# Performance work log

Hardware: AMD Instinct MI355X
Metric: run time of the kernel (lower is better)

## Reference

```python
import jax, jax.numpy as jnp
import numpy as np

D_MODEL = 1024
NUM_HEADS = 16
WINDOW = 128
DISP = WINDOW // 2
SHIFTED = True
NEG = -9e15


def _create_mask(w):
    # 1 = keep, 0 = masked; zero top-right and bottom-left DISP blocks
    m = np.ones((w, w), dtype=np.float32)
    m[:DISP, -DISP:] = 0.0
    m[-DISP:, :DISP] = 0.0
    return jnp.asarray(m)


def setup_inputs() -> dict:
    key = jax.random.key(0)
    ks = jax.random.split(key, 5)
    b, s, d = 4, 8192, D_MODEL
    sc = 1.0 / np.sqrt(d)
    return {
        "x": jax.random.normal(ks[0], (b, s, d), jnp.float32),
        "w_qkv": jax.random.normal(ks[1], (d, 3 * d), jnp.float32) * sc,
        "b_qkv": jax.random.normal(ks[2], (3 * d,), jnp.float32) * 0.02,
        "w_o": jax.random.normal(ks[3], (d, d), jnp.float32) * sc,
        "b_o": jax.random.normal(ks[4], (d,), jnp.float32) * 0.02,
    }


def reference(x, w_qkv, b_qkv, w_o, b_o):
    b, s, d = x.shape
    h, w = NUM_HEADS, WINDOW
    d_k = d // h
    if SHIFTED:
        x = jnp.roll(x, -DISP, axis=1)
    xw = x.reshape(-1, w, d)                       # (n, w, d), n = b*s/w
    n = xw.shape[0]
    qkv = xw @ w_qkv + b_qkv                       # (n, w, 3d)
    # replicate torch rearrange 'n w (h d_k qkv) -> n h w (d_k qkv)' + chunk(3)
    qkv = qkv.reshape(n, w, h, d_k, 3)             # split (h d_k qkv)
    qkv = qkv.transpose(0, 2, 1, 3, 4).reshape(n, h, w, 3 * d_k)
    q, k, v = jnp.split(qkv, 3, axis=-1)           # each (n, h, w, d_k)
    attn = jnp.einsum('nhqd,nhkd->nhqk', q, k) / jnp.sqrt(jnp.float32(d_k))
    if SHIFTED:
        mask = _create_mask(w)                     # (w, w)
        attn = jnp.where(mask == 0, jnp.float32(NEG), attn)
    attn = jax.nn.softmax(attn, axis=-1)
    vals = jnp.einsum('nhqk,nhkd->nhqd', attn, v)  # (n, h, w, d_k)
    vals = vals.transpose(0, 2, 1, 3).reshape(n, w, d)
    out = vals @ w_o + b_o                         # (n, w, d)
    out = out.reshape(b, s, d)
    if SHIFTED:
        out = jnp.roll(out, DISP, axis=1)
    return out
```

## Files before the change

### kernel.cpp

```cpp
#include <hip/hip_runtime.h>
#include <hip/hip_bf16.h>
#include <stdint.h>

#define D_MODEL   1024
#define SEQ       8192
#define BATCH     4
#define ROWS      (BATCH*SEQ)
#define NQKV      3072
#define HEADS     16
#define DKH       64

typedef _Float16 f16;
typedef f16   f16x8 __attribute__((ext_vector_type(8)));
typedef f16   f16x4 __attribute__((ext_vector_type(4)));
typedef float f32x4 __attribute__((ext_vector_type(4)));

#define AS1 __attribute__((address_space(1)))
#define AS3 __attribute__((address_space(3)))

__device__ __forceinline__ void lds_load16(const void* g, void* l) {
  __builtin_amdgcn_global_load_lds((const AS1 void*)g, (AS3 void*)l, 16, 0, 0);
}

__global__ void cvt_weights(const float* __restrict__ wqkv,
                            const float* __restrict__ bqkv,
                            const float* __restrict__ wo,
                            f16* __restrict__ wqkvT,
                            float* __restrict__ bqkvR,
                            f16* __restrict__ woT)
{
  const int NW1 = NQKV * D_MODEL;
  const int NW2 = D_MODEL * D_MODEL;
  int i = blockIdx.x * 256 + threadIdx.x;
  if (i < NW1) {
    int c = i % NQKV, k = i / NQKV;
    int hh = c / 192, rr = c % 192;
    int t  = rr >> 6, a = rr & 63;
    int n  = t * 1024 + hh * 64 + a;
    wqkvT[(size_t)n * 1024 + k] = (f16)wqkv[i];
  } else if (i < NW1 + NW2) {
    int j = i - NW1;
    int n = j % D_MODEL, k = j / D_MODEL;
    woT[(size_t)n * 1024 + k] = (f16)wo[j];
  } else if (i < NW1 + NW2 + NQKV) {
    int c = i - NW1 - NW2;
    int hh = c / 192, rr = c % 192;
    int t  = rr >> 6, a = rr & 63;
    bqkvR[t * 1024 + hh * 64 + a] = bqkv[c];
  }
}

__global__ void cvt_x(const float* __restrict__ x, f16* __restrict__ xb)
{
  int i  = blockIdx.x * 256 + threadIdx.x;
  int r  = i >> 7;
  int c8 = i & 127;
  int bb = r >> 13, p = r & 8191;
  int sr = (bb << 13) | ((p + 64) & 8191);
  const float* src = x + (size_t)sr * 1024 + c8 * 8;
  float4 v0 = *(const float4*)(src);
  float4 v1 = *(const float4*)(src + 4);
  f16x8 o = { (f16)v0.x, (f16)v0.y, (f16)v0.z, (f16)v0.w,
              (f16)v1.x, (f16)v1.y, (f16)v1.z, (f16)v1.w };
  *(f16x8*)(xb + (size_t)r * 1024 + c8 * 8) = o;
}

template<int EPI>
__global__ __launch_bounds__(256)
void gemm_bt(const f16* __restrict__ A, const f16* __restrict__ B,
             const float* __restrict__ bias,
             f16* __restrict__ outQ, f16* __restrict__ outK,
             f16* __restrict__ outVT, float* __restrict__ outF,
             int Ntiles)
{
  __shared__ alignas(16) char lds[32768];
  char* Asm = lds;
  char* Bsm = lds + 16384;

  int nwg  = gridDim.x;
  int cpx  = nwg >> 3;
  int work = (blockIdx.x & 7) * cpx + (blockIdx.x >> 3);
  int mt = work / Ntiles, nt = work % Ntiles;
  int m0 = mt * 128, n0 = nt * 128;

  int tid = threadIdx.x;
  int w = tid >> 6, l = tid & 63;
  int wr = w >> 1, wc = w & 1;
  int srow = l >> 3, sj = l & 7;
  int c16 = l & 15, g4 = l >> 4;

  const char* Ab = (const char*)A;
  const char* Bb = (const char*)B;

  f32x4 acc[4][4];
#pragma unroll
  for (int mi = 0; mi < 4; ++mi)
#pragma unroll
    for (int nj = 0; nj < 4; ++nj)
      acc[mi][nj] = (f32x4){0.f, 0.f, 0.f, 0.f};

  for (int kt = 0; kt < 16; ++kt) {
    int k0 = kt * 64;
#pragma unroll
    for (int q = 0; q < 4; ++q) {
      int r  = w * 32 + q * 8 + srow;
      int jg = sj ^ (r & 7);
      lds_load16(Ab + (size_t)(m0 + r) * 2048 + k0 * 2 + jg * 16,
                 Asm + (w * 32 + q * 8) * 128);
      lds_load16(Bb + (size_t)(n0 + r) * 2048 + k0 * 2 + jg * 16,
                 Bsm + (w * 32 + q * 8) * 128);
    }
    __syncthreads();
#pragma unroll
    for (int kk = 0; kk < 2; ++kk) {
      f16x8 af[4], bfr[4];
#pragma unroll
      for (int mi = 0; mi < 4; ++mi) {
        int r  = wr * 64 + mi * 16 + c16;
        int ch = ((kk << 2) | g4) ^ (r & 7);
        af[mi] = *(const f16x8*)(Asm + r * 128 + ch * 16);
      }
#pragma unroll
      for (int nj = 0; nj < 4; ++nj) {
        int r  = wc * 64 + nj * 16 + c16;
        int ch = ((kk << 2) | g4) ^ (r & 7);
        bfr[nj] = *(const f16x8*)(Bsm + r * 128 + ch * 16);
      }
#pragma unroll
      for (int mi = 0; mi < 4; ++mi)
#pragma unroll
        for (int nj = 0; nj < 4; ++nj)
          acc[mi][nj] = __builtin_amdgcn_mfma_f32_16x16x32_f16(
              af[mi], bfr[nj], acc[mi][nj], 0, 0, 0);
    }
    __syncthreads();
  }

  int rbase = g4 * 4;
  if (EPI == 0) {
    int tt = n0 >> 10;
#pragma unroll
    for (int mi = 0; mi < 4; ++mi) {
#pragma unroll
      for (int nj = 0; nj < 4; ++nj) {
        int n  = n0 + wc * 64 + nj * 16 + c16;
        int nn = n & 1023;
        float bv = bias[n];
#pragma unroll
        for (int j = 0; j < 4; ++j) {
          int m = m0 + wr * 64 + mi * 16 + rbase + j;
          float v = acc[mi][nj][j] + bv;
          if (tt == 0) {
            outQ[(size_t)m * 1024 + nn] = (f16)v;
          } else if (tt == 1) {
            outK[(size_t)m * 1024 + nn] = (f16)v;
          } else {
            int sub = m >> 6, key = m & 63;
            int hh = nn >> 6, dk = nn & 63;
            outVT[(((size_t)(sub * 16 + hh) * 64 + dk) << 6) + key] = (f16)v;
          }
        }
      }
    }
  } else {
#pragma unroll
    for (int mi = 0; mi < 4; ++mi) {
#pragma unroll
      for (int nj = 0; nj < 4; ++nj) {
        int n = n0 + wc * 64 + nj * 16 + c16;
        float bv = bias[n];
#pragma unroll
        for (int j = 0; j < 4; ++j) {
          int m = m0 + wr * 64 + mi * 16 + rbase + j;
          int bb = m >> 13, p = m & 8191;
          int dr = (bb << 13) | ((p + 64) & 8191);
          outF[(size_t)dr * 1024 + n] = acc[mi][nj][j] + bv;
        }
      }
    }
  }
}

__global__ __launch_bounds__(64)
void attn64(const f16* __restrict__ Q, const f16* __restrict__ Kb,
            const f16* __restrict__ VT, f16* __restrict__ O)
{
  __shared__ alignas(16) char plds[8192];
  int u = blockIdx.x;
  int sub = u >> 4, hh = u & 15;
  int l = threadIdx.x;
  int c = l & 15, g = l >> 4;

  const char* Qb = (const char*)Q  + (size_t)sub * 64 * 2048 + hh * 128;
  const char* KB = (const char*)Kb + (size_t)sub * 64 * 2048 + hh * 128;
  const char* VB = (const char*)VT + (size_t)u * 8192;

  f16x8 aq[4][2], bk[4][2];
#pragma unroll
  for (int mi = 0; mi < 4; ++mi)
#pragma unroll
    for (int kb = 0; kb < 2; ++kb)
      aq[mi][kb] = *(const f16x8*)(Qb + (mi * 16 + c) * 2048 + (kb * 32 + g * 8) * 2);
#pragma unroll
  for (int nj = 0; nj < 4; ++nj)
#pragma unroll
    for (int kb = 0; kb < 2; ++kb)
      bk[nj][kb] = *(const f16x8*)(KB + (nj * 16 + c) * 2048 + (kb * 32 + g * 8) * 2);

  f32x4 s[4][4];
#pragma unroll
  for (int mi = 0; mi < 4; ++mi)
#pragma unroll
    for (int nj = 0; nj < 4; ++nj)
      s[mi][nj] = (f32x4){0.f, 0.f, 0.f, 0.f};
#pragma unroll
  for (int kb = 0; kb < 2; ++kb)
#pragma unroll
    for (int mi = 0; mi < 4; ++mi)
#pragma unroll
      for (int nj = 0; nj < 4; ++nj)
        s[mi][nj] = __builtin_amdgcn_mfma_f32_16x16x32_f16(
            aq[mi][kb], bk[nj][kb], s[mi][nj], 0, 0, 0);

  const float SM_SCALE = 0.125f * 1.44269504089f;
#pragma unroll
  for (int mi = 0; mi < 4; ++mi) {
#pragma unroll
    for (int j = 0; j < 4; ++j) {
      float v0 = s[mi][0][j], v1 = s[mi][1][j], v2 = s[mi][2][j], v3 = s[mi][3][j];
      float mx = fmaxf(fmaxf(v0, v1), fmaxf(v2, v3));
      mx = fmaxf(mx, __shfl_xor(mx, 1));
      mx = fmaxf(mx, __shfl_xor(mx, 2));
      mx = fmaxf(mx, __shfl_xor(mx, 4));
      mx = fmaxf(mx, __shfl_xor(mx, 8));
      float p0 = exp2f((v0 - mx) * SM_SCALE);
      float p1 = exp2f((v1 - mx) * SM_SCALE);
      float p2 = exp2f((v2 - mx) * SM_SCALE);
      float p3 = exp2f((v3 - mx) * SM_SCALE);
      float sm = (p0 + p1) + (p2 + p3);
      sm += __shfl_xor(sm, 1);
      sm += __shfl_xor(sm, 2);
      sm += __shfl_xor(sm, 4);
      sm += __shfl_xor(sm, 8);
      float inv = 1.0f / sm;
      int r = mi * 16 + g * 4 + j;
      int rbyte = r * 128, rx = (r & 7) << 4;
      {
        int key = c;
        *(f16*)(plds + rbyte + (((key >> 3) << 4) ^ rx) + ((key & 7) << 1)) = (f16)(p0 * inv);
      }
      {
        int key = 16 + c;
        *(f16*)(plds + rbyte + (((key >> 3) << 4) ^ rx) + ((key & 7) << 1)) = (f16)(p1 * inv);
      }
      {
        int key = 32 + c;
        *(f16*)(plds + rbyte + (((key >> 3) << 4) ^ rx) + ((key & 7) << 1)) = (f16)(p2 * inv);
      }
      {
        int key = 48 + c;
        *(f16*)(plds + rbyte + (((key >> 3) << 4) ^ rx) + ((key & 7) << 1)) = (f16)(p3 * inv);
      }
    }
  }
  __syncthreads();

  f16x8 ap[4][2], bv[4][2];
#pragma unroll
  for (int mi = 0; mi < 4; ++mi) {
    int rowq = mi * 16 + c;
    int base = rowq * 128, rx = rowq & 7;
#pragma unroll
    for (int kb = 0; kb < 2; ++kb) {
      int ch = ((kb << 2) | g) ^ rx;
      ap[mi][kb] = *(const f16x8*)(plds + base + (ch << 4));
    }
  }
#pragma unroll
  for (int nj = 0; nj < 4; ++nj) {
    int dk = nj * 16 + c;
#pragma unroll
    for (int kb = 0; kb < 2; ++kb)
      bv[nj][kb] = *(const f16x8*)(VB + (dk * 64 + kb * 32 + g * 8) * 2);
  }

  f32x4 o[4][4];
#pragma unroll
  for (int mi = 0; mi < 4; ++mi)
#pragma unroll
    for (int nj = 0; nj < 4; ++nj)
      o[mi][nj] = (f32x4){0.f, 0.f, 0.f, 0.f};
#pragma unroll
  for (int kb = 0; kb < 2; ++kb)
#pragma unroll
    for (int mi = 0; mi < 4; ++mi)
#pragma unroll
      for (int nj = 0; nj < 4; ++nj)
        o[mi][nj] = __builtin_amdgcn_mfma_f32_16x16x32_f16(
            ap[mi][kb], bv[nj][kb], o[mi][nj], 0, 0, 0);

#pragma unroll
  for (int mi = 0; mi < 4; ++mi)
#pragma unroll
    for (int nj = 0; nj < 4; ++nj)
#pragma unroll
      for (int j = 0; j < 4; ++j) {
        int qrow = mi * 16 + g * 4 + j;
        int dk = nj * 16 + c;
        O[(size_t)(sub * 64 + qrow) * 1024 + hh * 64 + dk] = (f16)o[mi][nj][j];
      }
}

extern "C" void kernel_launch(void* const* d_in, const int* in_sizes, int n_in,
                              void* d_out, int out_size, void* d_ws, size_t ws_size,
                              hipStream_t stream)
{
  const float* x    = (const float*)d_in[0];
  const float* wqkv = (const float*)d_in[1];
  const float* bqkv = (const float*)d_in[2];
  const float* wo   = (const float*)d_in[3];
  const float* bo   = (const float*)d_in[4];
  float* out = (float*)d_out;
  char* ws = (char*)d_ws;

  f16*   xb    = (f16*)(ws + 0);
  f16*   wqkvT = (f16*)(ws + 67108864);
  float* bqkvR = (float*)(ws + 73400320);
  f16*   woT   = (f16*)(ws + 73412608);
  f16*   Qb    = (f16*)(ws + 75509760);
  f16*   Kb    = (f16*)(ws + 142618624);
  f16*   VTb   = (f16*)(ws + 209727488);
  f16*   A2    = (f16*)(ws + 0);

  cvt_weights<<<16396, 256, 0, stream>>>(wqkv, bqkv, wo, wqkvT, bqkvR, woT);
  cvt_x<<<16384, 256, 0, stream>>>(x, xb);
  gemm_bt<0><<<6144, 256, 0, stream>>>(xb, wqkvT, bqkvR, Qb, Kb, VTb, nullptr, 24);
  attn64<<<8192, 64, 0, stream>>>(Qb, Kb, VTb, A2);
  gemm_bt<1><<<2048, 256, 0, stream>>>(A2, woT, bo, nullptr, nullptr, nullptr, out, 8);
}
```

Baseline: 768.2 us.

## Replace GEMMs with 256x256 8-wave double-buffered pipelined MFMA kernel

Rewrites both projection GEMMs to use 256x256 output tiles with 8 waves and 128KB of double-buffered LDS. Global-to-LDS loads for the next k-step are interleaved with MFMA quadrants, using explicit waitcnt and barriers plus setprio around the MFMA bursts. The goal is more data reuse per tile and hiding load latency behind compute. In exchange it uses more registers and LDS, which lowers occupancy, and the grids become smaller: 1536 and 512 workgroups.

Result: faster. 665.6 us (-13.4%).

```diff
diff --git a/kernel.cpp b/kernel.cpp
--- a/kernel.cpp
+++ b/kernel.cpp
@@ -5,10 +5,8 @@
 #define D_MODEL   1024
 #define SEQ       8192
 #define BATCH     4
-#define ROWS      (BATCH*SEQ)
 #define NQKV      3072
 #define HEADS     16
-#define DKH       64
 
 typedef _Float16 f16;
 typedef f16   f16x8 __attribute__((ext_vector_type(8)));
@@ -65,91 +63,115 @@
   *(f16x8*)(xb + (size_t)r * 1024 + c8 * 8) = o;
 }
 
+#define BARX() { asm volatile("" ::: "memory"); __builtin_amdgcn_s_barrier(); \
+                 __builtin_amdgcn_sched_barrier(0); }
+
+#define LOADA(d,qm) { _Pragma("unroll") for (int mi=0;mi<4;++mi){ \
+    int rr = wm*64 + mi*16 + c16; \
+    const char* p = lds + (d)*65536 + (qm)*16384 + rr*128; \
+    _Pragma("unroll") for (int ks=0;ks<2;++ks) \
+      a[mi][ks] = *(const f16x8*)(p + ((((ks<<2)|g4) ^ (rr&7))<<4)); } }
+
+#define LOADB(d,qn) { _Pragma("unroll") for (int nj=0;nj<2;++nj){ \
+    int rr = wn*32 + nj*16 + c16; \
+    const char* p = lds + (d)*65536 + 32768 + (qn)*16384 + rr*128; \
+    _Pragma("unroll") for (int ks=0;ks<2;++ks) \
+      b[nj][ks] = *(const f16x8*)(p + ((((ks<<2)|g4) ^ (rr&7))<<4)); } }
+
+#define MF16(qm,qn) { __builtin_amdgcn_s_setprio(1); \
+    _Pragma("unroll") for (int mi=0;mi<4;++mi) \
+    _Pragma("unroll") for (int nj=0;nj<2;++nj){ \
+      acc[(qm)*4+mi][(qn)*2+nj] = __builtin_amdgcn_mfma_f32_16x16x32_f16( \
+          a[mi][0], b[nj][0], acc[(qm)*4+mi][(qn)*2+nj], 0,0,0); \
+      acc[(qm)*4+mi][(qn)*2+nj] = __builtin_amdgcn_mfma_f32_16x16x32_f16( \
+          a[mi][1], b[nj][1], acc[(qm)*4+mi][(qn)*2+nj], 0,0,0); } \
+    __builtin_amdgcn_s_setprio(0); }
+
 template<int EPI>
-__global__ __launch_bounds__(256)
-void gemm_bt(const f16* __restrict__ A, const f16* __restrict__ B,
-             const float* __restrict__ bias,
-             f16* __restrict__ outQ, f16* __restrict__ outK,
-             f16* __restrict__ outVT, float* __restrict__ outF,
-             int Ntiles)
-{
-  __shared__ alignas(16) char lds[32768];
-  char* Asm = lds;
-  char* Bsm = lds + 16384;
+__global__ __launch_bounds__(512, 2)
+void gemm8(const f16* __restrict__ A, const f16* __restrict__ B,
+           const float* __restrict__ bias,
+           f16* __restrict__ outQ, f16* __restrict__ outK,
+           f16* __restrict__ outVT, float* __restrict__ outF,
+           int Ntiles)
+{
+  __shared__ alignas(16) char lds[131072];
 
   int nwg  = gridDim.x;
-  int cpx  = nwg >> 3;
-  int work = (blockIdx.x & 7) * cpx + (blockIdx.x >> 3);
+  int work = ((int)blockIdx.x & 7) * (nwg >> 3) + ((int)blockIdx.x >> 3);
   int mt = work / Ntiles, nt = work % Ntiles;
-  int m0 = mt * 128, n0 = nt * 128;
+  int m0 = mt * 256, n0 = nt * 256;
 
   int tid = threadIdx.x;
-  int w = tid >> 6, l = tid & 63;
-  int wr = w >> 1, wc = w & 1;
-  int srow = l >> 3, sj = l & 7;
-  int c16 = l & 15, g4 = l >> 4;
-
-  const char* Ab = (const char*)A;
-  const char* Bb = (const char*)B;
-
-  f32x4 acc[4][4];
-#pragma unroll
-  for (int mi = 0; mi < 4; ++mi)
-#pragma unroll
-    for (int nj = 0; nj < 4; ++nj)
-      acc[mi][nj] = (f32x4){0.f, 0.f, 0.f, 0.f};
-
-  for (int kt = 0; kt < 16; ++kt) {
-    int k0 = kt * 64;
-#pragma unroll
-    for (int q = 0; q < 4; ++q) {
-      int r  = w * 32 + q * 8 + srow;
-      int jg = sj ^ (r & 7);
-      lds_load16(Ab + (size_t)(m0 + r) * 2048 + k0 * 2 + jg * 16,
-                 Asm + (w * 32 + q * 8) * 128);
-      lds_load16(Bb + (size_t)(n0 + r) * 2048 + k0 * 2 + jg * 16,
-                 Bsm + (w * 32 + q * 8) * 128);
-    }
-    __syncthreads();
-#pragma unroll
-    for (int kk = 0; kk < 2; ++kk) {
-      f16x8 af[4], bfr[4];
-#pragma unroll
-      for (int mi = 0; mi < 4; ++mi) {
-        int r  = wr * 64 + mi * 16 + c16;
-        int ch = ((kk << 2) | g4) ^ (r & 7);
-        af[mi] = *(const f16x8*)(Asm + r * 128 + ch * 16);
-      }
-#pragma unroll
-      for (int nj = 0; nj < 4; ++nj) {
-        int r  = wc * 64 + nj * 16 + c16;
-        int ch = ((kk << 2) | g4) ^ (r & 7);
-        bfr[nj] = *(const f16x8*)(Bsm + r * 128 + ch * 16);
-      }
-#pragma unroll
-      for (int mi = 0; mi < 4; ++mi)
-#pragma unroll
-        for (int nj = 0; nj < 4; ++nj)
-          acc[mi][nj] = __builtin_amdgcn_mfma_f32_16x16x32_f16(
-              af[mi], bfr[nj], acc[mi][nj], 0, 0, 0);
-    }
-    __syncthreads();
-  }
-
-  int rbase = g4 * 4;
+  int w = tid >> 6, lane = tid & 63;
+  int wm = w >> 2, wn = w & 3;
+  int c16 = lane & 15, g4 = lane >> 4;
+
+  int rr0 = tid >> 3;
+  int sc  = (((tid & 7) ^ ((tid >> 3) & 7)) << 4);
+  const char* pA = (const char*)A + (size_t)(m0 + rr0) * 2048 + sc;
+  const char* pB = (const char*)B + (size_t)(n0 + ((rr0 >> 5) << 6) + (rr0 & 31)) * 2048 + sc;
+  char* dstA = lds + w * 1024;
+  char* dstB = lds + 32768 + w * 1024;
+
+  auto stageA = [&](int d, int qm, int t) {
+    const char* s = pA + (size_t)(qm * 64) * 2048 + (size_t)t * 128;
+    lds_load16(s,              dstA + d * 65536 + qm * 16384);
+    lds_load16(s + 128 * 2048, dstA + d * 65536 + qm * 16384 + 8192);
+  };
+  auto stageB = [&](int d, int qn, int t) {
+    const char* s = pB + (size_t)(qn * 32) * 2048 + (size_t)t * 128;
+    lds_load16(s,              dstB + d * 65536 + qn * 16384);
+    lds_load16(s + 128 * 2048, dstB + d * 65536 + qn * 16384 + 8192);
+  };
+
+  f32x4 acc[8][4];
+#pragma unroll
+  for (int i = 0; i < 8; ++i)
+#pragma unroll
+    for (int j = 0; j < 4; ++j)
+      acc[i][j] = (f32x4){0.f, 0.f, 0.f, 0.f};
+  f16x8 a[4][2], b[2][2];
+
+  stageA(0, 0, 0); stageB(0, 0, 0); stageA(0, 1, 0); stageB(0, 1, 0);
+  stageA(1, 0, 1); stageB(1, 0, 1);
+  asm volatile("s_waitcnt vmcnt(4)" ::: "memory");
+  BARX();
+
+  for (int t = 0; t < 16; ++t) {
+    int d = t & 1, e = d ^ 1;
+    LOADA(d, 0); LOADB(d, 0);
+    if (t < 15) stageA(e, 1, t + 1);
+    BARX(); MF16(0, 0); BARX();
+    LOADB(d, 1);
+    if (t < 15) stageB(e, 1, t + 1);
+    BARX(); MF16(0, 1); BARX();
+    LOADA(d, 1); LOADB(d, 0);
+    if (t < 14) stageA(d, 0, t + 2);
+    BARX(); MF16(1, 0); BARX();
+    LOADB(d, 1);
+    if (t < 14) {
+      stageB(d, 0, t + 2);
+      asm volatile("s_waitcnt vmcnt(4)" ::: "memory");
+    } else if (t == 14) {
+      asm volatile("s_waitcnt vmcnt(0)" ::: "memory");
+    }
+    BARX(); MF16(1, 1); BARX();
+  }
+
   if (EPI == 0) {
     int tt = n0 >> 10;
 #pragma unroll
-    for (int mi = 0; mi < 4; ++mi) {
-#pragma unroll
-      for (int nj = 0; nj < 4; ++nj) {
-        int n  = n0 + wc * 64 + nj * 16 + c16;
+    for (int ai = 0; ai < 8; ++ai) {
+#pragma unroll
+      for (int bj = 0; bj < 4; ++bj) {
+        int n  = n0 + wn * 64 + bj * 16 + c16;
         int nn = n & 1023;
         float bv = bias[n];
 #pragma unroll
         for (int j = 0; j < 4; ++j) {
-          int m = m0 + wr * 64 + mi * 16 + rbase + j;
-          float v = acc[mi][nj][j] + bv;
+          int m = m0 + wm * 128 + ai * 16 + g4 * 4 + j;
+          float v = acc[ai][bj][j] + bv;
           if (tt == 0) {
             outQ[(size_t)m * 1024 + nn] = (f16)v;
           } else if (tt == 1) {
@@ -164,17 +186,17 @@
     }
   } else {
 #pragma unroll
-    for (int mi = 0; mi < 4; ++mi) {
-#pragma unroll
-      for (int nj = 0; nj < 4; ++nj) {
-        int n = n0 + wc * 64 + nj * 16 + c16;
+    for (int ai = 0; ai < 8; ++ai) {
+#pragma unroll
+      for (int bj = 0; bj < 4; ++bj) {
+        int n = n0 + wn * 64 + bj * 16 + c16;
         float bv = bias[n];
 #pragma unroll
         for (int j = 0; j < 4; ++j) {
-          int m = m0 + wr * 64 + mi * 16 + rbase + j;
+          int m = m0 + wm * 128 + ai * 16 + g4 * 4 + j;
           int bb = m >> 13, p = m & 8191;
           int dr = (bb << 13) | ((p + 64) & 8191);
-          outF[(size_t)dr * 1024 + n] = acc[mi][nj][j] + bv;
+          outF[(size_t)dr * 1024 + n] = acc[ai][bj][j] + bv;
         }
       }
     }
@@ -334,7 +356,7 @@
 
   cvt_weights<<<16396, 256, 0, stream>>>(wqkv, bqkv, wo, wqkvT, bqkvR, woT);
   cvt_x<<<16384, 256, 0, stream>>>(x, xb);
-  gemm_bt<0><<<6144, 256, 0, stream>>>(xb, wqkvT, bqkvR, Qb, Kb, VTb, nullptr, 24);
+  gemm8<0><<<1536, 512, 0, stream>>>(xb, wqkvT, bqkvR, Qb, Kb, VTb, nullptr, 12);
   attn64<<<8192, 64, 0, stream>>>(Qb, Kb, VTb, A2);
-  gemm_bt<1><<<2048, 256, 0, stream>>>(A2, woT, bo, nullptr, nullptr, nullptr, out, 8);
-}
+  gemm8<1><<<512, 512, 0, stream>>>(A2, woT, bo, nullptr, nullptr, nullptr, out, 4);
+}
```
